# Kernel optimization log

Measured on AMD Instinct MI355X. Metric: run time of the kernel, lower is better.

Reference implementation:

```python
import jax, jax.numpy as jnp
import numpy as np

N = 100000      # nodes
E = 1600000     # edges (avg degree 16)
D_IN = 128
D_H = 128
D_OUT = 2


def setup_inputs() -> dict:
    key = jax.random.key(0)
    ks = jax.random.split(key, 13)
    s = 0.05
    x = jax.random.normal(ks[0], (N, D_IN), jnp.float32)
    edge_src = jax.random.randint(ks[1], (E,), 0, N, jnp.int32)
    edge_dst = jax.random.randint(ks[2], (E,), 0, N, jnp.int32)
    # SAGEConv params per layer: lin_l (aggregated path, with bias), lin_r (root path)
    w_l0 = jax.random.normal(ks[3], (D_H, D_IN), jnp.float32) * s
    b0 = jnp.zeros((D_H,), jnp.float32)
    w_r0 = jax.random.normal(ks[4], (D_H, D_IN), jnp.float32) * s
    w_l1 = jax.random.normal(ks[5], (D_H, D_H), jnp.float32) * s
    b1 = jnp.zeros((D_H,), jnp.float32)
    w_r1 = jax.random.normal(ks[6], (D_H, D_H), jnp.float32) * s
    w_l2 = jax.random.normal(ks[7], (D_OUT, D_H), jnp.float32) * s
    b2 = jnp.zeros((D_OUT,), jnp.float32)
    w_r2 = jax.random.normal(ks[8], (D_OUT, D_H), jnp.float32) * s
    return {"x": x, "w_l0": w_l0, "b0": b0, "w_r0": w_r0,
            "w_l1": w_l1, "b1": b1, "w_r1": w_r1,
            "w_l2": w_l2, "b2": b2, "w_r2": w_r2,
            "edge_src": edge_src, "edge_dst": edge_dst}


def _sage_conv(h, src, dst, inv_deg, w_l, b, w_r):
    # mean aggregation of neighbor features: gather -> segment_sum -> scale
    agg = jax.ops.segment_sum(h[src], dst, num_segments=N) * inv_deg  # [N, d_in]
    return agg @ w_l.T + b + h @ w_r.T


def reference(x, w_l0, b0, w_r0, w_l1, b1, w_r1, w_l2, b2, w_r2, edge_src, edge_dst):
    # in-degree for mean aggregation (0-degree nodes -> mean of 0)
    deg = jax.ops.segment_sum(jnp.ones((E,), jnp.float32), edge_dst, num_segments=N)
    inv_deg = (1.0 / jnp.maximum(deg, 1.0))[:, None]  # [N, 1]
    h = jax.nn.relu(_sage_conv(x, edge_src, edge_dst, inv_deg, w_l0, b0, w_r0))
    # dropout is identity at inference (training=False)
    h = jax.nn.relu(_sage_conv(h, edge_src, edge_dst, inv_deg, w_l1, b1, w_r1))
    out = _sage_conv(h, edge_src, edge_dst, inv_deg, w_l2, b2, w_r2)
    return jax.nn.log_softmax(out, axis=1)
```

## Files before the change

kernel.cpp:

```cpp
#include <hip/hip_runtime.h>
#include <stdint.h>
#include <stddef.h>

#define DH 128
#define CHUNK 4096
#define PBK_SHIFT 9
#define NBKMAX 224

typedef short v8s __attribute__((ext_vector_type(8)));
typedef float v4f __attribute__((ext_vector_type(4)));

static __device__ __forceinline__ float bf2f(uint16_t h) {
    union { uint32_t i; float f; } u; u.i = ((uint32_t)h) << 16; return u.f;
}
static __device__ __forceinline__ uint16_t f2bf(float f) {
    union { float f; uint32_t i; } u; u.f = f;
    uint32_t r = u.i + 0x7fffu + ((u.i >> 16) & 1u);
    return (uint16_t)(r >> 16);
}
static __device__ __forceinline__ float loadf(const void* p, size_t i, bool f32) {
    return f32 ? ((const float*)p)[i] : bf2f(((const uint16_t*)p)[i]);
}

__global__ void histA_k(const int* __restrict__ dst, const uint32_t* w, int* flag,
                        int* gh, int E, int n, int GH, int nbk) {
    __shared__ int h[NBKMAX];
    int t = threadIdx.x;
    if (blockIdx.x == 0 && t < 64) {
        int hits = 0;
        for (int k = 0; k < 4; ++k) {
            uint32_t u = w[t * 4 + k];
            int e = (u >> 7) & 0xFF;
            hits += (e >= 100 && e <= 130) ? 1 : 0;
        }
        for (int off = 32; off; off >>= 1) hits += __shfl_down(hits, off);
        if (t == 0) *flag = (hits >= 128) ? 0 : 1;
    }
    int base = blockIdx.x * CHUNK;
    for (int i = t; i < NBKMAX; i += 256) h[i] = 0;
    __syncthreads();
    for (int it = 0; it < CHUNK / 256; ++it) {
        int e = base + it * 256 + t;
        if (e < E) {
            int d = dst[e];
            if ((unsigned)d < (unsigned)n) atomicAdd(&h[d >> PBK_SHIFT], 1);
        }
    }
    __syncthreads();
    for (int b = t; b < nbk; b += 256) gh[b * GH + blockIdx.x] = h[b];
}

__global__ void cvtall_k(const void* x, const void* wl0, const void* wr0,
                         const void* wl1, const void* wr1, const void* b0,
                         const void* b1, const int* dt, uint16_t* xb,
                         uint16_t* wcvt, int nx) {
    int i = blockIdx.x * 256 + threadIdx.x;
    bool f32 = (*dt != 0);
    if (i < nx) {
        if (f32) xb[i] = f2bf(((const float*)x)[i]);
        return;
    }
    int j = i - nx;
    const void* src; int off;
    if      (j < 16384) { src = wl0; off = j; }
    else if (j < 32768) { src = wr0; off = j - 16384; }
    else if (j < 49152) { src = wl1; off = j - 32768; }
    else if (j < 65536) { src = wr1; off = j - 49152; }
    else if (j < 65664) { src = b0;  off = j - 65536; }
    else if (j < 65792) { src = b1;  off = j - 65664; }
    else return;
    wcvt[j] = f32 ? f2bf(((const float*)src)[off]) : ((const uint16_t*)src)[off];
}

__global__ void scan1_k(const int* cnt, int* bsum, int n) {
    __shared__ int wt[4];
    int t = threadIdx.x, lane = t & 63, wv = t >> 6;
    int i = blockIdx.x * 256 + t;
    int v = (i < n) ? cnt[i] : 0;
    for (int off = 32; off; off >>= 1) v += __shfl_down(v, off);
    if (lane == 0) wt[wv] = v;
    __syncthreads();
    if (t == 0) bsum[blockIdx.x] = wt[0] + wt[1] + wt[2] + wt[3];
}

__global__ void scan2_k(const int* bsum, int* boff, int* row_n, int nb) {
    __shared__ int wt[4];
    __shared__ int carry_s;
    int t = threadIdx.x, lane = t & 63, wv = t >> 6;
    if (t == 0) carry_s = 0;
    __syncthreads();
    for (int base = 0; base < nb; base += 256) {
        int i = base + t;
        int c = (i < nb) ? bsum[i] : 0;
        int v = c;
        for (int off = 1; off < 64; off <<= 1) {
            int u = __shfl_up(v, off);
            if (lane >= off) v += u;
        }
        if (lane == 63) wt[wv] = v;
        __syncthreads();
        int woff = 0;
        for (int w = 0; w < wv; ++w) woff += wt[w];
        int total = wt[0] + wt[1] + wt[2] + wt[3];
        int carry = carry_s;
        if (i < nb) boff[i] = carry + woff + (v - c);
        __syncthreads();
        if (t == 0) carry_s = carry + total;
        __syncthreads();
    }
    if (t == 0) *row_n = carry_s;
}

__global__ void scanG3_k(const int* in, const int* boff, int* out, int n) {
    __shared__ int wt[4];
    int t = threadIdx.x, lane = t & 63, wv = t >> 6;
    int i = blockIdx.x * 256 + t;
    int c = (i < n) ? in[i] : 0;
    int v = c;
    for (int off = 1; off < 64; off <<= 1) {
        int u = __shfl_up(v, off);
        if (lane >= off) v += u;
    }
    if (lane == 63) wt[wv] = v;
    __syncthreads();
    int woff = 0;
    for (int w = 0; w < wv; ++w) woff += wt[w];
    if (i < n) out[i] = boff[blockIdx.x] + woff + (v - c);
}

__global__ void scatB_k(const int* __restrict__ src, const int* __restrict__ dst,
                        const int* __restrict__ ghs, uint32_t* gbuf,
                        int E, int n, int GH, int nbk) {
    __shared__ int cur[NBKMAX];
    int t = threadIdx.x;
    int base = blockIdx.x * CHUNK;
    for (int b = t; b < nbk; b += 256) cur[b] = ghs[b * GH + blockIdx.x];
    __syncthreads();
    for (int it = 0; it < CHUNK / 256; ++it) {
        int e = base + it * 256 + t;
        if (e < E) {
            int d = dst[e];
            if ((unsigned)d < (unsigned)n) {
                int s = src[e];
                int slot = atomicAdd(&cur[d >> PBK_SHIFT], 1);
                uint32_t rec = ((uint32_t)(d & 511) << 17) | (uint32_t)s;
                __builtin_nontemporal_store(rec, &gbuf[slot]);
            }
        }
    }
}

__global__ void regroupC_k(const uint32_t* __restrict__ gbuf, const int* ghs,
                           const int* __restrict__ totalp, int GH,
                           int* row_start, float* inv_deg, int* csr_src,
                           int n, int nbk) {
    __shared__ int lcnt[512];
    __shared__ int rs[512];
    __shared__ int wsum[4];
    int b = blockIdx.x, t = threadIdx.x, lane = t & 63, wv = t >> 6;
    int node0 = b << PBK_SHIFT;
    int nn = n - node0; if (nn > 512) nn = 512;
    int start = ghs[b * GH];
    int end = (b + 1 < nbk) ? ghs[(b + 1) * GH] : *totalp;
    for (int i = t; i < 512; i += 256) lcnt[i] = 0;
    __syncthreads();
    for (int i = start + t; i < end; i += 256)
        atomicAdd(&lcnt[gbuf[i] >> 17], 1);
    __syncthreads();
    int c0 = lcnt[2 * t], c1 = lcnt[2 * t + 1];
    int s = c0 + c1;
    int v = s;
    for (int off = 1; off < 64; off <<= 1) {
        int u = __shfl_up(v, off);
        if (lane >= off) v += u;
    }
    if (lane == 63) wsum[wv] = v;
    __syncthreads();
    int woff = 0;
    for (int w = 0; w < wv; ++w) woff += wsum[w];
    int ex = woff + (v - s);
    rs[2 * t]     = ex;
    rs[2 * t + 1] = ex + c0;
    __syncthreads();
    for (int i = t; i < nn; i += 256) {
        row_start[node0 + i] = start + rs[i];
        inv_deg[node0 + i] = 1.0f / fmaxf((float)lcnt[i], 1.0f);
    }
    __syncthreads();
    for (int i = t; i < 512; i += 256) lcnt[i] = 0;
    __syncthreads();
    for (int i = start + t; i < end; i += 256) {
        uint32_t rec = gbuf[i];
        int local = rec >> 17;
        int sv = rec & 0x1FFFF;
        int rank = atomicAdd(&lcnt[local], 1);
        csr_src[start + rs[local] + rank] = sv;
    }
}

__global__ void agg_k(const uint16_t* feat, const uint16_t* feat_alt, const int* xdt,
                      const int* csr_src, const int* row_start, const float* inv_deg,
                      uint16_t* A, int n) {
    int wave = threadIdx.x >> 6, lane = threadIdx.x & 63;
    int node = blockIdx.x * 4 + wave;
    if (node >= n) return;
    const uint16_t* f = feat;
    if (xdt != nullptr && *xdt == 0) f = feat_alt;
    int seg = lane & 7, sub = lane >> 3;
    int e0 = row_start[node], e1 = row_start[node + 1];
    const uint4* fp = (const uint4*)f;
    float acc[16];
#pragma unroll
    for (int i = 0; i < 16; ++i) acc[i] = 0.f;
    for (int e = e0 + sub; e < e1; e += 8) {
        int s = csr_src[e];
        if ((unsigned)s >= (unsigned)n) continue;
        const uint4* row = fp + (size_t)s * 16 + seg * 2;
        uint4 u0 = row[0];
        uint4 u1 = row[1];
        acc[0]  += bf2f((uint16_t)u0.x); acc[1]  += bf2f((uint16_t)(u0.x >> 16));
        acc[2]  += bf2f((uint16_t)u0.y); acc[3]  += bf2f((uint16_t)(u0.y >> 16));
        acc[4]  += bf2f((uint16_t)u0.z); acc[5]  += bf2f((uint16_t)(u0.z >> 16));
        acc[6]  += bf2f((uint16_t)u0.w); acc[7]  += bf2f((uint16_t)(u0.w >> 16));
        acc[8]  += bf2f((uint16_t)u1.x); acc[9]  += bf2f((uint16_t)(u1.x >> 16));
        acc[10] += bf2f((uint16_t)u1.y); acc[11] += bf2f((uint16_t)(u1.y >> 16));
        acc[12] += bf2f((uint16_t)u1.z); acc[13] += bf2f((uint16_t)(u1.z >> 16));
        acc[14] += bf2f((uint16_t)u1.w); acc[15] += bf2f((uint16_t)(u1.w >> 16));
    }
#pragma unroll
    for (int i = 0; i < 16; ++i) {
        acc[i] += __shfl_down(acc[i], 32);
        acc[i] += __shfl_down(acc[i], 16);
        acc[i] += __shfl_down(acc[i], 8);
    }
    if (sub == 0) {
        float sc = inv_deg[node];
        uint4 o0, o1;
        o0.x = (uint32_t)f2bf(acc[0]*sc)  | ((uint32_t)f2bf(acc[1]*sc)  << 16);
        o0.y = (uint32_t)f2bf(acc[2]*sc)  | ((uint32_t)f2bf(acc[3]*sc)  << 16);
        o0.z = (uint32_t)f2bf(acc[4]*sc)  | ((uint32_t)f2bf(acc[5]*sc)  << 16);
        o0.w = (uint32_t)f2bf(acc[6]*sc)  | ((uint32_t)f2bf(acc[7]*sc)  << 16);
        o1.x = (uint32_t)f2bf(acc[8]*sc)  | ((uint32_t)f2bf(acc[9]*sc)  << 16);
        o1.y = (uint32_t)f2bf(acc[10]*sc) | ((uint32_t)f2bf(acc[11]*sc) << 16);
        o1.z = (uint32_t)f2bf(acc[12]*sc) | ((uint32_t)f2bf(acc[13]*sc) << 16);
        o1.w = (uint32_t)f2bf(acc[14]*sc) | ((uint32_t)f2bf(acc[15]*sc) << 16);
        uint4* dst = (uint4*)A + (size_t)node * 16 + seg * 2;
        dst[0] = o0;
        dst[1] = o1;
    }
}

__global__ void dense2_k(const uint16_t* __restrict__ X,
                         const uint16_t* __restrict__ Xalt, const int* xdt,
                         const uint16_t* __restrict__ A,
                         const uint16_t* __restrict__ Wr,
                         const uint16_t* __restrict__ Wl,
                         const uint16_t* __restrict__ bias,
                         uint16_t* __restrict__ H,
                         const void* wl2, const void* wr2, const int* wdt,
                         float* T, float* Q, int n) {
    const int lane = threadIdx.x & 63;
    const int wv = threadIdx.x >> 6;
    const int m0 = blockIdx.x * 128 + wv * 32;
    if (m0 >= n) return;
    const uint16_t* Xs = X;
    if (xdt != nullptr && *xdt == 0) Xs = Xalt;
    const bool tq = (T != nullptr);
    const bool wf = tq && (*wdt != 0);
    const int row16 = lane & 15, quad = lane >> 4;
    int mr0 = m0 + row16;      int ml0 = (mr0 < n) ? mr0 : (n - 1);
    int mr1 = m0 + 16 + row16; int ml1 = (mr1 < n) ? mr1 : (n - 1);
    v8s ax0[4], aa0[4], ax1[4], aa1[4];
    const uint16_t* xr0 = Xs + (size_t)ml0 * DH + quad * 8;
    const uint16_t* ar0 = A  + (size_t)ml0 * DH + quad * 8;
    const uint16_t* xr1 = Xs + (size_t)ml1 * DH + quad * 8;
    const uint16_t* ar1 = A  + (size_t)ml1 * DH + quad * 8;
#pragma unroll
    for (int kt = 0; kt < 4; ++kt) {
        ax0[kt] = *(const v8s*)(xr0 + kt * 32);
        aa0[kt] = *(const v8s*)(ar0 + kt * 32);
        ax1[kt] = *(const v8s*)(xr1 + kt * 32);
        aa1[kt] = *(const v8s*)(ar1 + kt * 32);
    }
    float tqa[4][8];
    if (tq) {
#pragma unroll
        for (int a = 0; a < 4; ++a)
#pragma unroll
            for (int j = 0; j < 8; ++j) tqa[a][j] = 0.f;
    }
#pragma unroll
    for (int nt = 0; nt < 8; ++nt) {
        v4f acc0 = {0.f, 0.f, 0.f, 0.f};
        v4f acc1 = {0.f, 0.f, 0.f, 0.f};
        const uint16_t* wrr = Wr + (size_t)(nt * 16 + row16) * DH + quad * 8;
        const uint16_t* wlr = Wl + (size_t)(nt * 16 + row16) * DH + quad * 8;
#pragma unroll
        for (int kt = 0; kt < 4; ++kt) {
            v8s br = *(const v8s*)(wrr + kt * 32);
            acc0 = __builtin_amdgcn_mfma_f32_16x16x32_bf16(ax0[kt], br, acc0, 0, 0, 0);
            acc1 = __builtin_amdgcn_mfma_f32_16x16x32_bf16(ax1[kt], br, acc1, 0, 0, 0);
            v8s bl = *(const v8s*)(wlr + kt * 32);
            acc0 = __builtin_amdgcn_mfma_f32_16x16x32_bf16(aa0[kt], bl, acc0, 0, 0, 0);
            acc1 = __builtin_amdgcn_mfma_f32_16x16x32_bf16(aa1[kt], bl, acc1, 0, 0, 0);
        }
        int o = nt * 16 + row16;
        float bo = bf2f(bias[o]);
        float wl2_0 = 0.f, wl2_1 = 0.f, wr2_0 = 0.f, wr2_1 = 0.f;
        if (tq) {
            wl2_0 = loadf(wl2, o, wf);  wl2_1 = loadf(wl2, 128 + o, wf);
            wr2_0 = loadf(wr2, o, wf);  wr2_1 = loadf(wr2, 128 + o, wf);
        }
#pragma unroll
        for (int r = 0; r < 4; ++r) {
            int m = m0 + quad * 4 + r;
            float h0 = fmaxf(acc0[r] + bo, 0.0f);
            if (m < n) H[(size_t)m * DH + o] = f2bf(h0);
            int m2 = m0 + 16 + quad * 4 + r;
            float h1 = fmaxf(acc1[r] + bo, 0.0f);
            if (m2 < n) H[(size_t)m2 * DH + o] = f2bf(h1);
            if (tq) {
                tqa[0][r] += h0 * wl2_0; tqa[1][r] += h0 * wl2_1;
                tqa[2][r] += h0 * wr2_0; tqa[3][r] += h0 * wr2_1;
                tqa[0][4 + r] += h1 * wl2_0; tqa[1][4 + r] += h1 * wl2_1;
                tqa[2][4 + r] += h1 * wr2_0; tqa[3][4 + r] += h1 * wr2_1;
            }
        }
    }
    if (tq) {
#pragma unroll
        for (int mbit = 1; mbit < 16; mbit <<= 1)
#pragma unroll
            for (int a = 0; a < 4; ++a)
#pragma unroll
                for (int j = 0; j < 8; ++j)
                    tqa[a][j] += __shfl_xor(tqa[a][j], mbit);
        if (row16 == 0) {
#pragma unroll
            for (int r = 0; r < 4; ++r) {
                int m = m0 + quad * 4 + r;
                if (m < n) {
                    T[(size_t)m * 2]     = tqa[0][r];
                    T[(size_t)m * 2 + 1] = tqa[1][r];
                    Q[(size_t)m * 2]     = tqa[2][r];
                    Q[(size_t)m * 2 + 1] = tqa[3][r];
                }
                int m2 = m0 + 16 + quad * 4 + r;
                if (m2 < n) {
                    T[(size_t)m2 * 2]     = tqa[0][4 + r];
                    T[(size_t)m2 * 2 + 1] = tqa[1][4 + r];
                    Q[(size_t)m2 * 2]     = tqa[2][4 + r];
                    Q[(size_t)m2 * 2 + 1] = tqa[3][4 + r];
                }
            }
        }
    }
}

__global__ void final_k(const float* T, const float* Q, const int* row_start,
                        const int* csr_src, const float* inv_deg,
                        const void* b2, const int* wdt, float* out, int n) {
    int i = blockIdx.x * 256 + threadIdx.x;
    if (i >= n) return;
    bool f32 = (*wdt != 0);
    int e0 = row_start[i], e1 = row_start[i + 1];
    float s0 = 0.f, s1 = 0.f;
    const float2* T2 = (const float2*)T;
    for (int e = e0; e < e1; ++e) {
        int j = csr_src[e];
        if ((unsigned)j >= (unsigned)n) continue;
        float2 tv = T2[j];
        s0 += tv.x;
        s1 += tv.y;
    }
    float sc = inv_deg[i];
    float l0 = s0 * sc + loadf(b2, 0, f32) + Q[(size_t)i * 2];
    float l1 = s1 * sc + loadf(b2, 1, f32) + Q[(size_t)i * 2 + 1];
    float m = fmaxf(l0, l1);
    float lse = m + logf(expf(l0 - m) + expf(l1 - m));
    out[(size_t)i * 2]     = l0 - lse;
    out[(size_t)i * 2 + 1] = l1 - lse;
}

extern "C" void kernel_launch(void* const* d_in, const int* in_sizes, int n_in,
                              void* d_out, int out_size, void* d_ws, size_t ws_size,
                              hipStream_t stream) {
    int ix, iwl0, ib0, iwr0, iwl1, ib1, iwr1, iwl2, ib2, iwr2, iesrc, iedst;
    if (in_sizes[0] < 100000) {
        ib0 = 0; ib1 = 1; ib2 = 2; iedst = 3; iesrc = 4;
        iwl0 = 5; iwl1 = 6; iwl2 = 7; iwr0 = 8; iwr1 = 9; iwr2 = 10; ix = 11;
    } else {
        ix = 0; iwl0 = 1; ib0 = 2; iwr0 = 3; iwl1 = 4; ib1 = 5;
        iwr1 = 6; iwl2 = 7; ib2 = 8; iwr2 = 9; iesrc = 10; iedst = 11;
    }
    const void* x   = d_in[ix];
    const void* wl0 = d_in[iwl0];
    const void* b0  = d_in[ib0];
    const void* wr0 = d_in[iwr0];
    const void* wl1 = d_in[iwl1];
    const void* b1  = d_in[ib1];
    const void* wr1 = d_in[iwr1];
    const void* wl2 = d_in[iwl2];
    const void* b2  = d_in[ib2];
    const void* wr2 = d_in[iwr2];
    const int* esrc = (const int*)d_in[iesrc];
    const int* edst = (const int*)d_in[iedst];
    const int N = out_size / 2;
    const int E = in_sizes[iesrc];
    (void)n_in; (void)ws_size;

    char* ws = (char*)d_ws;
    size_t off = 0;
    auto carve = [&](size_t bytes) -> char* {
        char* p = ws + off;
        off = (off + bytes + 255) & ~(size_t)255;
        return p;
    };
    int gN = (N + 255) / 256;
    int GH = (E + CHUNK - 1) / CHUNK;
    int nbk = (N + 511) >> PBK_SHIFT;
    int n_scan = nbk * GH;
    int gS = (n_scan + 255) / 256;
    int* dtf        = (int*)   carve(256);
    int* gh         = (int*)   carve((size_t)n_scan * 4);
    int* ghs        = (int*)   carve((size_t)n_scan * 4);
    int* bsum       = (int*)   carve((size_t)gS * 4);
    int* boff       = (int*)   carve((size_t)gS * 4);
    uint32_t* gbuf  = (uint32_t*)carve((size_t)E * 4);
    int* row_start  = (int*)   carve((size_t)(N + 1) * 4);
    float* inv_deg  = (float*) carve((size_t)N * 4);
    int* csr_src    = (int*)   carve((size_t)E * 4);
    uint16_t* A16   = (uint16_t*)carve((size_t)N * DH * 2);
    uint16_t* H16   = (uint16_t*)carve((size_t)N * DH * 2);
    uint16_t* xb    = (uint16_t*)carve((size_t)N * DH * 2);
    uint16_t* wcvt  = (uint16_t*)carve(65792 * 2);
    float* T        = (float*) carve((size_t)N * 2 * 4);
    float* Q        = (float*) carve((size_t)N * 2 * 4);
    uint16_t* wl0b = wcvt;
    uint16_t* wr0b = wcvt + 16384;
    uint16_t* wl1b = wcvt + 32768;
    uint16_t* wr1b = wcvt + 49152;
    uint16_t* b0b  = wcvt + 65536;
    uint16_t* b1b  = wcvt + 65664;

    int ga = (N + 3) / 4;
    int gd = (N + 127) / 128;
    int nx = N * DH;
    int gc = (nx + 65792 + 255) / 256;

    histA_k<<<GH, 256, 0, stream>>>(edst, (const uint32_t*)wl0, dtf, gh, E, N, GH, nbk);
    cvtall_k<<<gc, 256, 0, stream>>>(x, wl0, wr0, wl1, wr1, b0, b1, dtf,
                                     xb, wcvt, nx);

    scan1_k<<<gS, 256, 0, stream>>>(gh, bsum, n_scan);
    scan2_k<<<1, 256, 0, stream>>>(bsum, boff, &row_start[N], gS);
    scanG3_k<<<gS, 256, 0, stream>>>(gh, boff, ghs, n_scan);
    scatB_k<<<GH, 256, 0, stream>>>(esrc, edst, ghs, gbuf, E, N, GH, nbk);
    regroupC_k<<<nbk, 256, 0, stream>>>(gbuf, ghs, &row_start[N], GH,
                                        row_start, inv_deg, csr_src, N, nbk);

    agg_k<<<ga, 256, 0, stream>>>(xb, (const uint16_t*)x, dtf,
                                  csr_src, row_start, inv_deg, A16, N);
    dense2_k<<<gd, 256, 0, stream>>>(xb, (const uint16_t*)x, dtf,
                                     A16, wr0b, wl0b, b0b, H16,
                                     nullptr, nullptr, nullptr,
                                     nullptr, nullptr, N);

    agg_k<<<ga, 256, 0, stream>>>(H16, nullptr, nullptr,
                                  csr_src, row_start, inv_deg, A16, N);
    dense2_k<<<gd, 256, 0, stream>>>(H16, nullptr, nullptr,
                                     A16, wr1b, wl1b, b1b, H16,
                                     wl2, wr2, dtf, T, Q, N);

    final_k<<<gN, 256, 0, stream>>>(T, Q, row_start, csr_src, inv_deg,
                                    b2, dtf, (float*)d_out, N);
}
```

Before: 464.4 us.

## Gather neighbor features from FP8 copies in aggregation kernels

Measured after the change: 470.4 us. No clear change (+1.3%).

```diff
diff --git a/kernel.cpp b/kernel.cpp
--- a/kernel.cpp
+++ b/kernel.cpp
@@ -9,6 +9,7 @@
 
 typedef short v8s __attribute__((ext_vector_type(8)));
 typedef float v4f __attribute__((ext_vector_type(4)));
+typedef float v2f __attribute__((ext_vector_type(2)));
 
 static __device__ __forceinline__ float bf2f(uint16_t h) {
     union { uint32_t i; float f; } u; u.i = ((uint32_t)h) << 16; return u.f;
@@ -20,6 +21,12 @@
 }
 static __device__ __forceinline__ float loadf(const void* p, size_t i, bool f32) {
     return f32 ? ((const float*)p)[i] : bf2f(((const uint16_t*)p)[i]);
+}
+static __device__ __forceinline__ uint16_t pack_fp8x2(float a, float b) {
+    return (uint16_t)(__builtin_amdgcn_cvt_pk_fp8_f32(a, b, 0, false) & 0xFFFF);
+}
+static __device__ __forceinline__ uint8_t pack_fp8(float a) {
+    return (uint8_t)(__builtin_amdgcn_cvt_pk_fp8_f32(a, 0.0f, 0, false) & 0xFF);
 }
 
 __global__ void histA_k(const int* __restrict__ dst, const uint32_t* w, int* flag,
@@ -53,14 +60,23 @@
 __global__ void cvtall_k(const void* x, const void* wl0, const void* wr0,
                          const void* wl1, const void* wr1, const void* b0,
                          const void* b1, const int* dt, uint16_t* xb,
-                         uint16_t* wcvt, int nx) {
+                         uint16_t* xq8, uint16_t* wcvt, int nxh) {
     int i = blockIdx.x * 256 + threadIdx.x;
     bool f32 = (*dt != 0);
-    if (i < nx) {
-        if (f32) xb[i] = f2bf(((const float*)x)[i]);
+    if (i < nxh) {
+        float v0, v1;
+        if (f32) {
+            const float2 v = ((const float2*)x)[i];
+            v0 = v.x; v1 = v.y;
+            ((uint32_t*)xb)[i] = (uint32_t)f2bf(v0) | ((uint32_t)f2bf(v1) << 16);
+        } else {
+            uint32_t u = ((const uint32_t*)x)[i];
+            v0 = bf2f((uint16_t)u); v1 = bf2f((uint16_t)(u >> 16));
+        }
+        xq8[i] = pack_fp8x2(v0, v1);
         return;
     }
-    int j = i - nx;
+    int j = i - nxh;
     const void* src; int off;
     if      (j < 16384) { src = wl0; off = j; }
     else if (j < 32768) { src = wr0; off = j - 16384; }
@@ -198,34 +214,30 @@
     }
 }
 
-__global__ void agg_k(const uint16_t* feat, const uint16_t* feat_alt, const int* xdt,
-                      const int* csr_src, const int* row_start, const float* inv_deg,
-                      uint16_t* A, int n) {
+__global__ void agg_k(const uint8_t* __restrict__ feat8,
+                      const int* csr_src, const int* row_start,
+                      const float* inv_deg, uint16_t* A, int n) {
     int wave = threadIdx.x >> 6, lane = threadIdx.x & 63;
     int node = blockIdx.x * 4 + wave;
     if (node >= n) return;
-    const uint16_t* f = feat;
-    if (xdt != nullptr && *xdt == 0) f = feat_alt;
     int seg = lane & 7, sub = lane >> 3;
     int e0 = row_start[node], e1 = row_start[node + 1];
-    const uint4* fp = (const uint4*)f;
     float acc[16];
 #pragma unroll
     for (int i = 0; i < 16; ++i) acc[i] = 0.f;
     for (int e = e0 + sub; e < e1; e += 8) {
         int s = csr_src[e];
         if ((unsigned)s >= (unsigned)n) continue;
-        const uint4* row = fp + (size_t)s * 16 + seg * 2;
-        uint4 u0 = row[0];
-        uint4 u1 = row[1];
-        acc[0]  += bf2f((uint16_t)u0.x); acc[1]  += bf2f((uint16_t)(u0.x >> 16));
-        acc[2]  += bf2f((uint16_t)u0.y); acc[3]  += bf2f((uint16_t)(u0.y >> 16));
-        acc[4]  += bf2f((uint16_t)u0.z); acc[5]  += bf2f((uint16_t)(u0.z >> 16));
-        acc[6]  += bf2f((uint16_t)u0.w); acc[7]  += bf2f((uint16_t)(u0.w >> 16));
-        acc[8]  += bf2f((uint16_t)u1.x); acc[9]  += bf2f((uint16_t)(u1.x >> 16));
-        acc[10] += bf2f((uint16_t)u1.y); acc[11] += bf2f((uint16_t)(u1.y >> 16));
-        acc[12] += bf2f((uint16_t)u1.z); acc[13] += bf2f((uint16_t)(u1.z >> 16));
-        acc[14] += bf2f((uint16_t)u1.w); acc[15] += bf2f((uint16_t)(u1.w >> 16));
+        uint4 u = *(const uint4*)(feat8 + (size_t)s * 128 + seg * 16);
+        v2f p;
+        p = __builtin_amdgcn_cvt_pk_f32_fp8(u.x, false); acc[0]  += p.x; acc[1]  += p.y;
+        p = __builtin_amdgcn_cvt_pk_f32_fp8(u.x, true);  acc[2]  += p.x; acc[3]  += p.y;
+        p = __builtin_amdgcn_cvt_pk_f32_fp8(u.y, false); acc[4]  += p.x; acc[5]  += p.y;
+        p = __builtin_amdgcn_cvt_pk_f32_fp8(u.y, true);  acc[6]  += p.x; acc[7]  += p.y;
+        p = __builtin_amdgcn_cvt_pk_f32_fp8(u.z, false); acc[8]  += p.x; acc[9]  += p.y;
+        p = __builtin_amdgcn_cvt_pk_f32_fp8(u.z, true);  acc[10] += p.x; acc[11] += p.y;
+        p = __builtin_amdgcn_cvt_pk_f32_fp8(u.w, false); acc[12] += p.x; acc[13] += p.y;
+        p = __builtin_amdgcn_cvt_pk_f32_fp8(u.w, true);  acc[14] += p.x; acc[15] += p.y;
     }
 #pragma unroll
     for (int i = 0; i < 16; ++i) {
@@ -257,6 +269,7 @@
                          const uint16_t* __restrict__ Wl,
                          const uint16_t* __restrict__ bias,
                          uint16_t* __restrict__ H,
+                         uint8_t* __restrict__ Hq8,
                          const void* wl2, const void* wr2, const int* wdt,
                          float* T, float* Q, int n) {
     const int lane = threadIdx.x & 63;
@@ -315,15 +328,22 @@
         for (int r = 0; r < 4; ++r) {
             int m = m0 + quad * 4 + r;
             float h0 = fmaxf(acc0[r] + bo, 0.0f);
-            if (m < n) H[(size_t)m * DH + o] = f2bf(h0);
             int m2 = m0 + 16 + quad * 4 + r;
             float h1 = fmaxf(acc1[r] + bo, 0.0f);
-            if (m2 < n) H[(size_t)m2 * DH + o] = f2bf(h1);
             if (tq) {
                 tqa[0][r] += h0 * wl2_0; tqa[1][r] += h0 * wl2_1;
                 tqa[2][r] += h0 * wr2_0; tqa[3][r] += h0 * wr2_1;
                 tqa[0][4 + r] += h1 * wl2_0; tqa[1][4 + r] += h1 * wl2_1;
                 tqa[2][4 + r] += h1 * wr2_0; tqa[3][4 + r] += h1 * wr2_1;
+            } else {
+                if (m < n) {
+                    H[(size_t)m * DH + o] = f2bf(h0);
+                    Hq8[(size_t)m * DH + o] = pack_fp8(h0);
+                }
+                if (m2 < n) {
+                    H[(size_t)m2 * DH + o] = f2bf(h1);
+                    Hq8[(size_t)m2 * DH + o] = pack_fp8(h1);
+                }
             }
         }
     }
@@ -433,6 +453,8 @@
     uint16_t* A16   = (uint16_t*)carve((size_t)N * DH * 2);
     uint16_t* H16   = (uint16_t*)carve((size_t)N * DH * 2);
     uint16_t* xb    = (uint16_t*)carve((size_t)N * DH * 2);
+    uint8_t*  xq8   = (uint8_t*) carve((size_t)N * DH);
+    uint8_t*  hq8   = (uint8_t*) carve((size_t)N * DH);
     uint16_t* wcvt  = (uint16_t*)carve(65792 * 2);
     float* T        = (float*) carve((size_t)N * 2 * 4);
     float* Q        = (float*) carve((size_t)N * 2 * 4);
@@ -445,12 +467,12 @@
 
     int ga = (N + 3) / 4;
     int gd = (N + 127) / 128;
-    int nx = N * DH;
-    int gc = (nx + 65792 + 255) / 256;
+    int nxh = (N * DH) / 2;
+    int gc = (nxh + 65792 + 255) / 256;
 
     histA_k<<<GH, 256, 0, stream>>>(edst, (const uint32_t*)wl0, dtf, gh, E, N, GH, nbk);
     cvtall_k<<<gc, 256, 0, stream>>>(x, wl0, wr0, wl1, wr1, b0, b1, dtf,
-                                     xb, wcvt, nx);
+                                     xb, (uint16_t*)xq8, wcvt, nxh);
 
     scan1_k<<<gS, 256, 0, stream>>>(gh, bsum, n_scan);
     scan2_k<<<1, 256, 0, stream>>>(bsum, boff, &row_start[N], gS);
@@ -459,17 +481,15 @@
     regroupC_k<<<nbk, 256, 0, stream>>>(gbuf, ghs, &row_start[N], GH,
                                         row_start, inv_deg, csr_src, N, nbk);
 
-    agg_k<<<ga, 256, 0, stream>>>(xb, (const uint16_t*)x, dtf,
-                                  csr_src, row_start, inv_deg, A16, N);
+    agg_k<<<ga, 256, 0, stream>>>(xq8, csr_src, row_start, inv_deg, A16, N);
     dense2_k<<<gd, 256, 0, stream>>>(xb, (const uint16_t*)x, dtf,
-                                     A16, wr0b, wl0b, b0b, H16,
+                                     A16, wr0b, wl0b, b0b, H16, hq8,
                                      nullptr, nullptr, nullptr,
                                      nullptr, nullptr, N);
 
-    agg_k<<<ga, 256, 0, stream>>>(H16, nullptr, nullptr,
-                                  csr_src, row_start, inv_deg, A16, N);
+    agg_k<<<ga, 256, 0, stream>>>(hq8, csr_src, row_start, inv_deg, A16, N);
     dense2_k<<<gd, 256, 0, stream>>>(H16, nullptr, nullptr,
-                                     A16, wr1b, wl1b, b1b, H16,
+                                     A16, wr1b, wl1b, b1b, nullptr, nullptr,
                                      wl2, wr2, dtf, T, Q, N);
 
     final_k<<<gN, 256, 0, stream>>>(T, Q, row_start, csr_src, inv_deg,
```
